# Optimization experiments

Measured on AMD Instinct MI355X. Metric: run time of the kernel, lower is better.

Reference implementation:

```python
import jax, jax.numpy as jnp
import numpy as np

B, C, H, W = 128, 32, 64, 64
L = H * W  # 4096
RATE = L * C  # 131072


def setup_inputs() -> dict:
    key = jax.random.key(0)
    k1, k2, k3, k4 = jax.random.split(key, 4)
    x = jax.random.normal(k1, (B, C, H, W), dtype=jnp.float32)
    px = jax.random.normal(k2, (1,), dtype=jnp.float32)
    # kaiming_normal_(a=sqrt(5)) on a (RATE, C) matrix: fan_in = C,
    # gain = sqrt(2/(1+a^2)) = sqrt(2/6), std = gain/sqrt(fan_in)
    std = np.sqrt(2.0 / 6.0) / np.sqrt(C)
    weight = jax.random.normal(k3, (RATE, C), dtype=jnp.float32) * std
    bound = 1.0 / np.sqrt(C)
    bias = jax.random.uniform(k4, (RATE,), dtype=jnp.float32, minval=-bound, maxval=bound)
    return {"x": x, "px": px, "weight": weight, "bias": bias}


def reference(x, px, weight, bias):
    b_, c_, h_, w_ = x.shape
    l_ = h_ * w_
    # [B, C, H, W] -> [B, L, C]
    x_blc = x.reshape(b_, c_, l_).transpose(0, 2, 1)
    w = weight.reshape(l_, c_, c_)   # per-position [C, C] weight
    b = bias.reshape(l_, c_)         # per-position bias
    # per-position batched matmul: (B,L,1,C) @ (L,C,C) -> (B,L,C)
    out = jnp.einsum('blc,lcd->bld', x_blc, w) + b
    # [B, L, C] -> [B, C, H, W]
    return out.reshape(b_, h_, w_, c_).transpose(0, 3, 1, 2)
```

## Files before the change

kernel.cpp:

```cpp
#include <hip/hip_runtime.h>
#include <stdint.h>


namespace {

constexpr int kC  = 32;
constexpr int kL  = 4096;
constexpr int kNB = 8;
constexpr int kND = 8;

__global__ __launch_bounds__(256, 4)
void dyna_dec(const float* __restrict__ x,
              const float* __restrict__ w,
              const float* __restrict__ bias,
              float* __restrict__ out) {
    const int lt = threadIdx.x & 63;
    const int dg = threadIdx.x >> 6;
    const int l  = blockIdx.x * 64 + lt;
    const int b0 = blockIdx.y * kNB;
    const int d0 = dg * kND;

    const float* wp = w + (size_t)l * (kC * kC) + d0;
    const float* xp = x + (size_t)b0 * (kC * kL) + l;

    float acc[kNB][kND];
#pragma unroll
    for (int i = 0; i < kNB; ++i)
#pragma unroll
        for (int j = 0; j < kND; ++j) acc[i][j] = 0.0f;

#pragma unroll 2
    for (int c = 0; c < kC; ++c) {
        const float4 w0 = *reinterpret_cast<const float4*>(wp + c * kC);
        const float4 w1 = *reinterpret_cast<const float4*>(wp + c * kC + 4);
        const float ws[kND] = {w0.x, w0.y, w0.z, w0.w, w1.x, w1.y, w1.z, w1.w};

        float xr[kNB];
#pragma unroll
        for (int i = 0; i < kNB; ++i)
            xr[i] = xp[(size_t)i * (kC * kL) + (size_t)c * kL];

#pragma unroll
        for (int i = 0; i < kNB; ++i)
#pragma unroll
            for (int j = 0; j < kND; ++j)
                acc[i][j] += xr[i] * ws[j];
    }

    const float4 b0v = *reinterpret_cast<const float4*>(bias + (size_t)l * kC + d0);
    const float4 b1v = *reinterpret_cast<const float4*>(bias + (size_t)l * kC + d0 + 4);
    const float bv[kND] = {b0v.x, b0v.y, b0v.z, b0v.w, b1v.x, b1v.y, b1v.z, b1v.w};

#pragma unroll
    for (int i = 0; i < kNB; ++i) {
        float* op = out + (size_t)(b0 + i) * (kC * kL) + l;
#pragma unroll
        for (int j = 0; j < kND; ++j)
            op[(size_t)(d0 + j) * kL] = acc[i][j] + bv[j];
    }
}

}

extern "C" void kernel_launch(void* const* d_in, const int* in_sizes, int n_in,
                              void* d_out, int out_size, void* d_ws, size_t ws_size,
                              hipStream_t stream) {
    const float* x    = (const float*)d_in[0];
    const float* wgt  = (const float*)d_in[2];
    const float* bias = (const float*)d_in[3];
    float* out = (float*)d_out;

    dim3 grid(kL / 64, 128 / kNB);
    dim3 block(256);
    hipLaunchKernelGGL(dyna_dec, grid, block, 0, stream, x, wgt, bias, out);
}
```

Baseline: 180.9 us.

## Stage weights through padded LDS with coalesced loads and prefetch x

The kernel now loads each block's 64-position weight slab cooperatively, four channels at a time, into padded shared memory using coalesced float4 reads. Previously each thread made strided per-thread global reads of 4 KB-spaced rows. It also double-buffers the x loads one channel ahead and writes output with nontemporal stores. The cost is 33 KB of LDS per block, which can cut occupancy under the 4-blocks launch bound, plus two barriers per chunk.

New measurement: 202.4 us. 11.9% more time.

```diff
diff --git a/kernel.cpp b/kernel.cpp
--- a/kernel.cpp
+++ b/kernel.cpp
@@ -4,24 +4,27 @@
 
 namespace {
 
-constexpr int kC  = 32;
-constexpr int kL  = 4096;
+constexpr int kC = 32;
+constexpr int kL = 4096;
 constexpr int kNB = 8;
 constexpr int kND = 8;
+constexpr int kCChunk = 4;
+constexpr int kRowPad = kCChunk * 32 + 4;
 
 __global__ __launch_bounds__(256, 4)
 void dyna_dec(const float* __restrict__ x,
               const float* __restrict__ w,
               const float* __restrict__ bias,
               float* __restrict__ out) {
-    const int lt = threadIdx.x & 63;
-    const int dg = threadIdx.x >> 6;
-    const int l  = blockIdx.x * 64 + lt;
+    __shared__ float sw[64 * kRowPad];
+
+    const int t  = threadIdx.x;
+    const int lt = t & 63;
+    const int dg = t >> 6;
+    const int lc = blockIdx.x * 64;
+    const int l  = lc + lt;
     const int b0 = blockIdx.y * kNB;
     const int d0 = dg * kND;
-
-    const float* wp = w + (size_t)l * (kC * kC) + d0;
-    const float* xp = x + (size_t)b0 * (kC * kL) + l;
 
     float acc[kNB][kND];
 #pragma unroll
@@ -29,34 +32,71 @@
 #pragma unroll
         for (int j = 0; j < kND; ++j) acc[i][j] = 0.0f;
 
-#pragma unroll 2
-    for (int c = 0; c < kC; ++c) {
-        const float4 w0 = *reinterpret_cast<const float4*>(wp + c * kC);
-        const float4 w1 = *reinterpret_cast<const float4*>(wp + c * kC + 4);
-        const float ws[kND] = {w0.x, w0.y, w0.z, w0.w, w1.x, w1.y, w1.z, w1.w};
+    const float* xp = x + (size_t)b0 * (kC * kL) + l;
 
-        float xr[kNB];
+    float xr[2][kNB];
 #pragma unroll
-        for (int i = 0; i < kNB; ++i)
-            xr[i] = xp[(size_t)i * (kC * kL) + (size_t)c * kL];
+    for (int i = 0; i < kNB; ++i)
+        xr[0][i] = xp[(size_t)i * (kC * kL)];
+
+    for (int k = 0; k < kC / kCChunk; ++k) {
+        const float* wsrc = w + ((size_t)lc * kC + k * kCChunk) * 32;
+#pragma unroll
+        for (int h = 0; h < 2; ++h) {
+            float4 tmp[4];
+#pragma unroll
+            for (int i = 0; i < 4; ++i) {
+                const int f4 = (h * 4 + i) * 256 + t;
+                const int lr = f4 >> 5;
+                const int m  = f4 & 31;
+                tmp[i] = *reinterpret_cast<const float4*>(
+                    wsrc + (size_t)lr * (kC * 32) + m * 4);
+            }
+#pragma unroll
+            for (int i = 0; i < 4; ++i) {
+                const int f4 = (h * 4 + i) * 256 + t;
+                const int lr = f4 >> 5;
+                const int m  = f4 & 31;
+                *reinterpret_cast<float4*>(&sw[lr * kRowPad + m * 4]) = tmp[i];
+            }
+        }
+        __syncthreads();
 
 #pragma unroll
-        for (int i = 0; i < kNB; ++i)
+        for (int cc = 0; cc < kCChunk; ++cc) {
+            const int c = k * kCChunk + cc;
+            if (c + 1 < kC) {
 #pragma unroll
-            for (int j = 0; j < kND; ++j)
-                acc[i][j] += xr[i] * ws[j];
+                for (int i = 0; i < kNB; ++i)
+                    xr[(c + 1) & 1][i] =
+                        xp[(size_t)i * (kC * kL) + (size_t)(c + 1) * kL];
+            }
+            const float4 wa = *reinterpret_cast<const float4*>(
+                &sw[lt * kRowPad + cc * 32 + d0]);
+            const float4 wb = *reinterpret_cast<const float4*>(
+                &sw[lt * kRowPad + cc * 32 + d0 + 4]);
+            const float ws[kND] = {wa.x, wa.y, wa.z, wa.w,
+                                   wb.x, wb.y, wb.z, wb.w};
+#pragma unroll
+            for (int i = 0; i < kNB; ++i)
+#pragma unroll
+                for (int j = 0; j < kND; ++j)
+                    acc[i][j] += xr[c & 1][i] * ws[j];
+        }
+        __syncthreads();
     }
 
-    const float4 b0v = *reinterpret_cast<const float4*>(bias + (size_t)l * kC + d0);
-    const float4 b1v = *reinterpret_cast<const float4*>(bias + (size_t)l * kC + d0 + 4);
-    const float bv[kND] = {b0v.x, b0v.y, b0v.z, b0v.w, b1v.x, b1v.y, b1v.z, b1v.w};
+    const float4 bv0 = *reinterpret_cast<const float4*>(bias + (size_t)l * kC + d0);
+    const float4 bv1 = *reinterpret_cast<const float4*>(bias + (size_t)l * kC + d0 + 4);
+    const float bb[kND] = {bv0.x, bv0.y, bv0.z, bv0.w,
+                           bv1.x, bv1.y, bv1.z, bv1.w};
 
 #pragma unroll
     for (int i = 0; i < kNB; ++i) {
-        float* op = out + (size_t)(b0 + i) * (kC * kL) + l;
+        float* op = out + ((size_t)(b0 + i) * kC + d0) * kL + l;
 #pragma unroll
         for (int j = 0; j < kND; ++j)
-            op[(size_t)(d0 + j) * kL] = acc[i][j] + bv[j];
+            __builtin_nontemporal_store(acc[i][j] + bb[j], op + (size_t)j * kL);
     }
 }
 
```

## Transpose weights to L-major layout in workspace and software-pipeline loads

Applied to the files above, without the earlier changes.

Adds a pre-pass kernel that transposes the per-position weight matrix into a [C*C, L] layout in the workspace, so the main kernel reads weights coalesced across adjacent positions instead of strided float4 gathers. The main kernel also double-buffers x and weight registers to prefetch the next channel. The cost is an extra 16 MB read plus 16 MB write and a second launch every call. The old gather kernel remains as a fallback when the workspace is too small.

After: 467.6 us. 158% more time.

```diff
diff --git a/kernel.cpp b/kernel.cpp
--- a/kernel.cpp
+++ b/kernel.cpp
@@ -6,21 +6,101 @@
 
 constexpr int kC  = 32;
 constexpr int kL  = 4096;
+constexpr int kCD = kC * kC;
 constexpr int kNB = 8;
 constexpr int kND = 8;
 
+__global__ __launch_bounds__(256)
+void transpose_w(const float* __restrict__ w, float* __restrict__ wt) {
+    __shared__ float tile[64][65];
+    const int tx = threadIdx.x & 63;
+    const int tg = threadIdx.x >> 6;
+    const int cd0 = blockIdx.x * 64;
+    const int l0  = blockIdx.y * 64;
+
+#pragma unroll
+    for (int k = 0; k < 16; ++k) {
+        const int r = tg * 16 + k;
+        tile[r][tx] = w[(size_t)(l0 + r) * kCD + cd0 + tx];
+    }
+    __syncthreads();
+#pragma unroll
+    for (int k = 0; k < 16; ++k) {
+        const int r = tg * 16 + k;
+        wt[(size_t)(cd0 + r) * kL + l0 + tx] = tile[tx][r];
+    }
+}
+
 __global__ __launch_bounds__(256, 4)
-void dyna_dec(const float* __restrict__ x,
-              const float* __restrict__ w,
-              const float* __restrict__ bias,
-              float* __restrict__ out) {
+void dyna_dec_t(const float* __restrict__ x,
+                const float* __restrict__ wt,
+                const float* __restrict__ bias,
+                float* __restrict__ out) {
     const int lt = threadIdx.x & 63;
     const int dg = threadIdx.x >> 6;
     const int l  = blockIdx.x * 64 + lt;
     const int b0 = blockIdx.y * kNB;
     const int d0 = dg * kND;
 
-    const float* wp = w + (size_t)l * (kC * kC) + d0;
+    const float* xp = x  + (size_t)b0 * (kC * kL) + l;
+    const float* wp = wt + (size_t)d0 * kL + l;
+
+    float acc[kNB][kND];
+#pragma unroll
+    for (int i = 0; i < kNB; ++i)
+#pragma unroll
+        for (int j = 0; j < kND; ++j) acc[i][j] = 0.0f;
+
+    float xr[2][kNB], wr[2][kND];
+#pragma unroll
+    for (int i = 0; i < kNB; ++i) xr[0][i] = xp[(size_t)i * (kC * kL)];
+#pragma unroll
+    for (int j = 0; j < kND; ++j) wr[0][j] = wp[(size_t)j * kL];
+
+#pragma unroll 4
+    for (int c = 0; c < kC; ++c) {
+        const int cur = c & 1, nxt = cur ^ 1;
+        if (c + 1 < kC) {
+#pragma unroll
+            for (int i = 0; i < kNB; ++i)
+                xr[nxt][i] = xp[(size_t)i * (kC * kL) + (size_t)(c + 1) * kL];
+#pragma unroll
+            for (int j = 0; j < kND; ++j)
+                wr[nxt][j] = wp[(size_t)((c + 1) * kC + j) * kL];
+        }
+#pragma unroll
+        for (int i = 0; i < kNB; ++i)
+#pragma unroll
+            for (int j = 0; j < kND; ++j)
+                acc[i][j] += xr[cur][i] * wr[cur][j];
+    }
+
+    const float4 bv0 = *reinterpret_cast<const float4*>(bias + (size_t)l * kC + d0);
+    const float4 bv1 = *reinterpret_cast<const float4*>(bias + (size_t)l * kC + d0 + 4);
+    const float bb[kND] = {bv0.x, bv0.y, bv0.z, bv0.w,
+                           bv1.x, bv1.y, bv1.z, bv1.w};
+
+#pragma unroll
+    for (int i = 0; i < kNB; ++i) {
+        float* op = out + ((size_t)(b0 + i) * kC + d0) * kL + l;
+#pragma unroll
+        for (int j = 0; j < kND; ++j)
+            op[(size_t)j * kL] = acc[i][j] + bb[j];
+    }
+}
+
+__global__ __launch_bounds__(256, 4)
+void dyna_dec_gather(const float* __restrict__ x,
+                     const float* __restrict__ w,
+                     const float* __restrict__ bias,
+                     float* __restrict__ out) {
+    const int lt = threadIdx.x & 63;
+    const int dg = threadIdx.x >> 6;
+    const int l  = blockIdx.x * 64 + lt;
+    const int b0 = blockIdx.y * kNB;
+    const int d0 = dg * kND;
+
+    const float* wp = w + (size_t)l * kCD + d0;
     const float* xp = x + (size_t)b0 * (kC * kL) + l;
 
     float acc[kNB][kND];
@@ -34,12 +114,10 @@
         const float4 w0 = *reinterpret_cast<const float4*>(wp + c * kC);
         const float4 w1 = *reinterpret_cast<const float4*>(wp + c * kC + 4);
         const float ws[kND] = {w0.x, w0.y, w0.z, w0.w, w1.x, w1.y, w1.z, w1.w};
-
         float xr[kNB];
 #pragma unroll
         for (int i = 0; i < kNB; ++i)
             xr[i] = xp[(size_t)i * (kC * kL) + (size_t)c * kL];
-
 #pragma unroll
         for (int i = 0; i < kNB; ++i)
 #pragma unroll
@@ -47,16 +125,16 @@
                 acc[i][j] += xr[i] * ws[j];
     }
 
-    const float4 b0v = *reinterpret_cast<const float4*>(bias + (size_t)l * kC + d0);
-    const float4 b1v = *reinterpret_cast<const float4*>(bias + (size_t)l * kC + d0 + 4);
-    const float bv[kND] = {b0v.x, b0v.y, b0v.z, b0v.w, b1v.x, b1v.y, b1v.z, b1v.w};
-
+    const float4 bv0 = *reinterpret_cast<const float4*>(bias + (size_t)l * kC + d0);
+    const float4 bv1 = *reinterpret_cast<const float4*>(bias + (size_t)l * kC + d0 + 4);
+    const float bb[kND] = {bv0.x, bv0.y, bv0.z, bv0.w,
+                           bv1.x, bv1.y, bv1.z, bv1.w};
 #pragma unroll
     for (int i = 0; i < kNB; ++i) {
-        float* op = out + (size_t)(b0 + i) * (kC * kL) + l;
+        float* op = out + ((size_t)(b0 + i) * kC + d0) * kL + l;
 #pragma unroll
         for (int j = 0; j < kND; ++j)
-            op[(size_t)(d0 + j) * kL] = acc[i][j] + bv[j];
+            op[(size_t)j * kL] = acc[i][j] + bb[j];
     }
 }
 
@@ -70,7 +148,15 @@
     const float* bias = (const float*)d_in[3];
     float* out = (float*)d_out;
 
-    dim3 grid(kL / 64, 128 / kNB);
-    dim3 block(256);
-    hipLaunchKernelGGL(dyna_dec, grid, block, 0, stream, x, wgt, bias, out);
+    const size_t wt_bytes = (size_t)kCD * kL * sizeof(float);
+    if (ws_size >= wt_bytes) {
+        float* wt = (float*)d_ws;
+        hipLaunchKernelGGL(transpose_w, dim3(kCD / 64, kL / 64), dim3(256),
+                           0, stream, wgt, wt);
+        hipLaunchKernelGGL(dyna_dec_t, dim3(kL / 64, 128 / kNB), dim3(256),
+                           0, stream, x, wt, bias, out);
+    } else {
+        hipLaunchKernelGGL(dyna_dec_gather, dim3(kL / 64, 128 / kNB), dim3(256),
+                           0, stream, x, wgt, bias, out);
+    }
 }
```
